# Kernel optimization log

Measured on AMD Instinct MI355X. Metric: run time of the kernel, lower is better.

Reference implementation:

```python
import jax, jax.numpy as jnp
import numpy as np

GAMMA = 10.0                      # self.gamma
MU = jnp.arange(0.0, 2.0, 0.1)    # self.mu_k, D=20
ORDER = 2                         # order arg to Stream


def setup_inputs() -> dict:
    key = jax.random.key(0)
    ks = jax.random.split(key, 6)
    B, N, F, D, Fv = 8, 512, 16, 20, 1
    coordinates = jax.random.uniform(ks[0], (B, N, 3), dtype=jnp.float32)
    atom_emb = jax.random.normal(ks[1], (1, 1, Fv), dtype=jnp.float32)   # xavier-style atom embedding
    W_e = jax.random.normal(ks[2], (D, F), dtype=jnp.float32) / np.sqrt(D)
    b_e = jnp.zeros((F,), jnp.float32)
    w_a = jax.random.normal(ks[3], (F,), dtype=jnp.float32) / np.sqrt(F)
    Wq = jax.random.normal(ks[4], (Fv, 1), dtype=jnp.float32)            # Q: Linear(F_v -> 1)
    bq = jnp.zeros((1,), jnp.float32)
    return dict(coordinates=coordinates, atom_emb=atom_emb, W_e=W_e,
                b_e=b_e, w_a=w_a, Wq=Wq, bq=bq)


def reference(coordinates, atom_emb, W_e, b_e, w_a, Wq, bq):
    B, N, _ = coordinates.shape
    # adjacency: pairwise Euclidean distances (B,N,N)
    diff = coordinates[:, :, None, :] - coordinates[:, None, :, :]
    d = jnp.sqrt(jnp.sum(diff * diff, axis=-1) + 1e-12)
    # rbf_expansion: Gaussian basis; original materializes (B,N,N,D) broadcasts
    rbf_d = jnp.exp(-GAMMA * (d[..., None] - MU) ** 2)   # (B,N,N,D)
    rbf_0 = jnp.exp(-GAMMA * MU ** 2)                    # (D,) basis at d=0 (constant over pairs)
    # geometric attention stream: edge features from RBF -> scalar attention
    feat_d = jnp.tanh(jnp.einsum('bnmd,df->bnmf', rbf_d, W_e) + b_e)  # (B,N,N,F)
    feat_0 = jnp.tanh(rbf_0 @ W_e + b_e)                              # (F,)
    # subtracting the d=0 baseline zeroes self-interaction on the diagonal
    alpha = jnp.einsum('bnmf,f->bnm', feat_d, w_a) - jnp.dot(feat_0, w_a)
    # message passing of order-k correlations over atom embeddings
    v = jnp.broadcast_to(atom_emb, (B, N, atom_emb.shape[-1]))  # (B,N,F_v)
    for _ in range(ORDER):
        v = v + jnp.einsum('bnm,bmf->bnf', alpha, v) / N
    # take stream output for node 0 and project: v_[:, 0, :] -> Q(.)
    return v[:, 0, :] @ Wq + bq  # (B,1)
```

## Files before the change

### kernel.cpp

```cpp
#include <hip/hip_runtime.h>
#include <math.h>


#define BB 8
#define NN 512
#define FF 16
#define DD 20
#define TBL 4096
#define DMAX 1.7320509f

__device__ __forceinline__ float eval_g(float d, const float* __restrict__ We,
                                        const float* __restrict__ be,
                                        const float* __restrict__ wa) {
    float z[FF];
#pragma unroll
    for (int f = 0; f < FF; ++f) z[f] = be[f];
#pragma unroll
    for (int k = 0; k < DD; ++k) {
        float u = d - 0.1f * (float)k;
        float r = __expf(-10.0f * u * u);
#pragma unroll
        for (int f = 0; f < FF; ++f) z[f] = fmaf(r, We[k * FF + f], z[f]);
    }
    float g = 0.0f;
#pragma unroll
    for (int f = 0; f < FF; ++f) g += wa[f] * tanhf(z[f]);
    return g;
}

__global__ void build_table(const float* __restrict__ We, const float* __restrict__ be,
                            const float* __restrict__ wa, float* __restrict__ tbl) {
    int i = blockIdx.x * blockDim.x + threadIdx.x;
    if (i <= TBL) {
        float d = (DMAX / (float)(TBL - 1)) * (float)i;
        tbl[i] = eval_g(d, We, be, wa);
    }
}

__global__ __launch_bounds__(256) void row_sums(const float* __restrict__ coords,
                                                const float* __restrict__ tbl,
                                                float* __restrict__ Srow) {
    __shared__ float sh[TBL + 1];
    for (int i = threadIdx.x; i <= TBL; i += 256) sh[i] = tbl[i];
    __syncthreads();

    const int wave = threadIdx.x >> 6;
    const int lane = threadIdx.x & 63;
    const int row  = blockIdx.x * 4 + wave;
    const int b = row >> 9;
    const int n = row & 511;
    const float* cb = coords + (size_t)b * NN * 3;
    const float cx = cb[n * 3 + 0], cy = cb[n * 3 + 1], cz = cb[n * 3 + 2];
    const float inv_h = (float)(TBL - 1) / DMAX;

    float acc = 0.0f;
    for (int m = lane; m < NN; m += 64) {
        float dx = cx - cb[m * 3 + 0];
        float dy = cy - cb[m * 3 + 1];
        float dz = cz - cb[m * 3 + 2];
        float dd = fmaf(dx, dx, fmaf(dy, dy, dz * dz)) + 1e-12f;
        float d  = sqrtf(dd);
        float x  = d * inv_h;
        int  i0  = (int)x;
        i0 = (i0 < TBL - 1) ? i0 : (TBL - 1);
        float fr = x - (float)i0;
        float t0 = sh[i0], t1 = sh[i0 + 1];
        acc += fmaf(fr, t1 - t0, t0);
    }
#pragma unroll
    for (int off = 32; off > 0; off >>= 1) acc += __shfl_down(acc, off, 64);
    if (lane == 0) Srow[row] = acc;
}

__global__ __launch_bounds__(512) void finalize(const float* __restrict__ coords,
                                                const float* __restrict__ tbl,
                                                const float* __restrict__ Srow,
                                                const float* __restrict__ atom_emb,
                                                const float* __restrict__ Wq,
                                                const float* __restrict__ bq,
                                                float* __restrict__ out) {
    __shared__ float sh[TBL + 1];
    __shared__ float red[NN];
    for (int i = threadIdx.x; i <= TBL; i += 512) sh[i] = tbl[i];
    __syncthreads();

    const int b = blockIdx.x;
    const int m = threadIdx.x;
    const float* cb = coords + (size_t)b * NN * 3;
    const float g0 = sh[0];
    const float a  = atom_emb[0];
    const float invN = 1.0f / (float)NN;

    float v1 = a * (1.0f + Srow[b * NN + m] * invN - g0);

    float dx = cb[0] - cb[m * 3 + 0];
    float dy = cb[1] - cb[m * 3 + 1];
    float dz = cb[2] - cb[m * 3 + 2];
    float dd = fmaf(dx, dx, fmaf(dy, dy, dz * dz)) + 1e-12f;
    float d  = sqrtf(dd);
    const float inv_h = (float)(TBL - 1) / DMAX;
    float x  = d * inv_h;
    int  i0  = (int)x;
    i0 = (i0 < TBL - 1) ? i0 : (TBL - 1);
    float fr = x - (float)i0;
    float al = fmaf(fr, sh[i0 + 1] - sh[i0], sh[i0]) - g0;

    red[m] = al * v1;
    __syncthreads();
    for (int s = 256; s > 0; s >>= 1) {
        if (m < s) red[m] += red[m + s];
        __syncthreads();
    }
    if (m == 0) {
        float v1_0 = a * (1.0f + Srow[b * NN + 0] * invN - g0);
        float v2_0 = v1_0 + red[0] * invN;
        out[b] = v2_0 * Wq[0] + bq[0];
    }
}

extern "C" void kernel_launch(void* const* d_in, const int* in_sizes, int n_in,
                              void* d_out, int out_size, void* d_ws, size_t ws_size,
                              hipStream_t stream) {
    const float* coords   = (const float*)d_in[0];
    const float* atom_emb = (const float*)d_in[1];
    const float* W_e      = (const float*)d_in[2];
    const float* b_e      = (const float*)d_in[3];
    const float* w_a      = (const float*)d_in[4];
    const float* Wq       = (const float*)d_in[5];
    const float* bq       = (const float*)d_in[6];
    float* out = (float*)d_out;

    float* tbl  = (float*)d_ws;
    float* Srow = tbl + (TBL + 16);

    build_table<<<(TBL + 1 + 255) / 256, 256, 0, stream>>>(W_e, b_e, w_a, tbl);
    row_sums<<<(BB * NN) / 4, 256, 0, stream>>>(coords, tbl, Srow);
    finalize<<<BB, 512, 0, stream>>>(coords, tbl, Srow, atom_emb, Wq, bq, out);
}
```

Baseline: 87.28 us.

## Fuse finalize into row-sum kernel via last-block atomic counter; halve table

Merges the row-sum and finalize kernels into one launch. A global atomic counter picks the last block to finish, and that block computes the node-0 reductions for all batches, which removes one kernel launch. The interpolation table is also halved to 2048 entries, which cuts the per-block shared-memory fill cost at the price of coarser interpolation. The serial tail now runs in a single 256-thread block, and correctness depends on the counter being reset in build_table each call.

```diff
diff --git a/kernel.cpp b/kernel.cpp
--- a/kernel.cpp
+++ b/kernel.cpp
@@ -6,8 +6,11 @@
 #define NN 512
 #define FF 16
 #define DD 20
-#define TBL 4096
+#define TBL 2048
 #define DMAX 1.7320509f
+
+#define WS_TBL_OFF 16
+#define WS_SROW_OFF (WS_TBL_OFF + TBL + 16)
 
 __device__ __forceinline__ float eval_g(float d, const float* __restrict__ We,
                                         const float* __restrict__ be,
@@ -29,23 +32,34 @@
 }
 
 __global__ void build_table(const float* __restrict__ We, const float* __restrict__ be,
-                            const float* __restrict__ wa, float* __restrict__ tbl) {
+                            const float* __restrict__ wa, float* __restrict__ ws) {
     int i = blockIdx.x * blockDim.x + threadIdx.x;
+    if (i == 0) ((int*)ws)[0] = 0;
     if (i <= TBL) {
         float d = (DMAX / (float)(TBL - 1)) * (float)i;
-        tbl[i] = eval_g(d, We, be, wa);
+        ws[WS_TBL_OFF + i] = eval_g(d, We, be, wa);
     }
 }
 
-__global__ __launch_bounds__(256) void row_sums(const float* __restrict__ coords,
-                                                const float* __restrict__ tbl,
-                                                float* __restrict__ Srow) {
+__global__ __launch_bounds__(256) void rows_finalize(const float* __restrict__ coords,
+                                                     float* __restrict__ ws,
+                                                     const float* __restrict__ atom_emb,
+                                                     const float* __restrict__ Wq,
+                                                     const float* __restrict__ bq,
+                                                     float* __restrict__ out) {
     __shared__ float sh[TBL + 1];
-    for (int i = threadIdx.x; i <= TBL; i += 256) sh[i] = tbl[i];
+    __shared__ float red[BB * 4];
+    __shared__ int is_last;
+    const float* tbl = ws + WS_TBL_OFF;
+    float* Srow = ws + WS_SROW_OFF;
+    int* cnt = (int*)ws;
+
+    const int tid = threadIdx.x;
+    for (int i = tid; i <= TBL; i += 256) sh[i] = tbl[i];
     __syncthreads();
 
-    const int wave = threadIdx.x >> 6;
-    const int lane = threadIdx.x & 63;
+    const int wave = tid >> 6;
+    const int lane = tid & 63;
     const int row  = blockIdx.x * 4 + wave;
     const int b = row >> 9;
     const int n = row & 511;
@@ -59,8 +73,7 @@
         float dy = cy - cb[m * 3 + 1];
         float dz = cz - cb[m * 3 + 2];
         float dd = fmaf(dx, dx, fmaf(dy, dy, dz * dz)) + 1e-12f;
-        float d  = sqrtf(dd);
-        float x  = d * inv_h;
+        float x  = sqrtf(dd) * inv_h;
         int  i0  = (int)x;
         i0 = (i0 < TBL - 1) ? i0 : (TBL - 1);
         float fr = x - (float)i0;
@@ -70,51 +83,52 @@
 #pragma unroll
     for (int off = 32; off > 0; off >>= 1) acc += __shfl_down(acc, off, 64);
     if (lane == 0) Srow[row] = acc;
-}
 
-__global__ __launch_bounds__(512) void finalize(const float* __restrict__ coords,
-                                                const float* __restrict__ tbl,
-                                                const float* __restrict__ Srow,
-                                                const float* __restrict__ atom_emb,
-                                                const float* __restrict__ Wq,
-                                                const float* __restrict__ bq,
-                                                float* __restrict__ out) {
-    __shared__ float sh[TBL + 1];
-    __shared__ float red[NN];
-    for (int i = threadIdx.x; i <= TBL; i += 512) sh[i] = tbl[i];
+    __threadfence();
     __syncthreads();
+    if (tid == 0) is_last = (atomicAdd(cnt, 1) == (int)gridDim.x - 1);
+    __syncthreads();
+    if (!is_last) return;
+    __threadfence();
 
-    const int b = blockIdx.x;
-    const int m = threadIdx.x;
-    const float* cb = coords + (size_t)b * NN * 3;
+    volatile const float* S = Srow;
     const float g0 = sh[0];
     const float a  = atom_emb[0];
     const float invN = 1.0f / (float)NN;
 
-    float v1 = a * (1.0f + Srow[b * NN + m] * invN - g0);
+    float accs[BB];
+#pragma unroll
+    for (int b2 = 0; b2 < BB; ++b2) accs[b2] = 0.0f;
 
-    float dx = cb[0] - cb[m * 3 + 0];
-    float dy = cb[1] - cb[m * 3 + 1];
-    float dz = cb[2] - cb[m * 3 + 2];
-    float dd = fmaf(dx, dx, fmaf(dy, dy, dz * dz)) + 1e-12f;
-    float d  = sqrtf(dd);
-    const float inv_h = (float)(TBL - 1) / DMAX;
-    float x  = d * inv_h;
-    int  i0  = (int)x;
-    i0 = (i0 < TBL - 1) ? i0 : (TBL - 1);
-    float fr = x - (float)i0;
-    float al = fmaf(fr, sh[i0 + 1] - sh[i0], sh[i0]) - g0;
-
-    red[m] = al * v1;
+    for (int b2 = 0; b2 < BB; ++b2) {
+        const float* c2 = coords + (size_t)b2 * NN * 3;
+        const float ox = c2[0], oy = c2[1], oz = c2[2];
+        for (int m = tid; m < NN; m += 256) {
+            float dx = ox - c2[m * 3 + 0];
+            float dy = oy - c2[m * 3 + 1];
+            float dz = oz - c2[m * 3 + 2];
+            float dd = fmaf(dx, dx, fmaf(dy, dy, dz * dz)) + 1e-12f;
+            float x  = sqrtf(dd) * inv_h;
+            int  i0  = (int)x;
+            i0 = (i0 < TBL - 1) ? i0 : (TBL - 1);
+            float fr = x - (float)i0;
+            float al = fmaf(fr, sh[i0 + 1] - sh[i0], sh[i0]) - g0;
+            float v1 = a * (1.0f + S[b2 * NN + m] * invN - g0);
+            accs[b2] = fmaf(al, v1, accs[b2]);
+        }
+    }
+#pragma unroll
+    for (int b2 = 0; b2 < BB; ++b2) {
+        float v = accs[b2];
+#pragma unroll
+        for (int off = 32; off > 0; off >>= 1) v += __shfl_down(v, off, 64);
+        if (lane == 0) red[b2 * 4 + wave] = v;
+    }
     __syncthreads();
-    for (int s = 256; s > 0; s >>= 1) {
-        if (m < s) red[m] += red[m + s];
-        __syncthreads();
-    }
-    if (m == 0) {
-        float v1_0 = a * (1.0f + Srow[b * NN + 0] * invN - g0);
-        float v2_0 = v1_0 + red[0] * invN;
-        out[b] = v2_0 * Wq[0] + bq[0];
+    if (tid < BB) {
+        float s = red[tid * 4 + 0] + red[tid * 4 + 1] + red[tid * 4 + 2] + red[tid * 4 + 3];
+        float v1_0 = a * (1.0f + S[tid * NN + 0] * invN - g0);
+        out[tid] = (v1_0 + s * invN) * Wq[0] + bq[0];
     }
 }
 
@@ -129,11 +143,8 @@
     const float* Wq       = (const float*)d_in[5];
     const float* bq       = (const float*)d_in[6];
     float* out = (float*)d_out;
+    float* ws  = (float*)d_ws;
 
-    float* tbl  = (float*)d_ws;
-    float* Srow = tbl + (TBL + 16);
-
-    build_table<<<(TBL + 1 + 255) / 256, 256, 0, stream>>>(W_e, b_e, w_a, tbl);
-    row_sums<<<(BB * NN) / 4, 256, 0, stream>>>(coords, tbl, Srow);
-    finalize<<<BB, 512, 0, stream>>>(coords, tbl, Srow, atom_emb, Wq, bq, out);
+    build_table<<<(TBL + 1 + 255) / 256, 256, 0, stream>>>(W_e, b_e, w_a, ws);
+    rows_finalize<<<(BB * NN) / 4, 256, 0, stream>>>(coords, ws, atom_emb, Wq, bq, out);
 }
```

Result: slower. 156.4 us (+79.2%).
